# Kernel tuning notes

Hardware: AMD Instinct MI355X
Metric: run time of the kernel (lower is better)

## Reference

```python
import jax, jax.numpy as jnp
import numpy as np

NUM_EMBEDDINGS = 1024
EMBEDDING_DIM = 64
BETA = 0.25


def setup_inputs() -> dict:
    key = jax.random.key(0)
    k1, k2 = jax.random.split(key)
    z = jax.random.normal(k1, (16, EMBEDDING_DIM, 64, 64), dtype=jnp.float32)
    # nn.Embedding weight initialized uniform(-1/K, 1/K)
    embedding = jax.random.uniform(
        k2, (NUM_EMBEDDINGS, EMBEDDING_DIM), dtype=jnp.float32,
        minval=-1.0 / NUM_EMBEDDINGS, maxval=1.0 / NUM_EMBEDDINGS)
    return {"z": z, "embedding": embedding}


def reference(z, embedding):
    # z: [B, C, H, W] -> [B, H, W, C]
    zp = jnp.transpose(z, (0, 2, 3, 1))
    B, H, W, C = zp.shape
    zf = zp.reshape(-1, C)  # [N, C]
    # squared euclidean distances to each codebook entry: [N, K]
    d = (jnp.sum(zf * zf, axis=1, keepdims=True)
         + jnp.sum(embedding * embedding, axis=1)
         - 2.0 * jnp.matmul(zf, embedding.T))
    train_indices = jnp.argmin(d, axis=1)  # [N]
    # gather codebook rows (mathematically identical to one-hot @ embedding)
    z_q = jnp.take(embedding, train_indices, axis=0).reshape(B, H, W, C)
    min_encodings = jax.nn.one_hot(train_indices, NUM_EMBEDDINGS, dtype=jnp.float32)
    embedding_loss = jnp.mean((jax.lax.stop_gradient(z_q) - zp) ** 2)
    q_latent_loss = jnp.mean((z_q - jax.lax.stop_gradient(zp)) ** 2)
    loss = q_latent_loss + BETA * embedding_loss
    # straight-through estimator
    z_q_st = zp + jax.lax.stop_gradient(z_q - zp)
    z_q_out = jnp.transpose(z_q_st, (0, 3, 1, 2))  # back to NCHW
    return loss, z_q_out, min_encodings, train_indices
```

## Files before the change

kernel.cpp:

```cpp
#include <hip/hip_runtime.h>
#include <float.h>


#define K_CODES 1024
#define DIM 64
#define NPTS 65536
#define RANGES 8
#define CPR 128
#define ZQ_OFF 1
#define OH_OFF (1 + 4194304)
#define IDX_OFF (1 + 4194304 + 67108864)
#define ZQ_N 4194304

__device__ __forceinline__ float np_sumsq64(const float* x) {
#pragma clang fp contract(off)
    float t[DIM];
#pragma unroll
    for (int c = 0; c < DIM; ++c) t[c] = x[c] * x[c];
    float r[8];
#pragma unroll
    for (int j = 0; j < 8; ++j) r[j] = t[j];
#pragma unroll
    for (int i = 8; i < DIM; i += 8)
#pragma unroll
        for (int j = 0; j < 8; ++j) r[j] += t[i + j];
    return ((r[0] + r[1]) + (r[2] + r[3])) + ((r[4] + r[5]) + (r[6] + r[7]));
}

__global__ __launch_bounds__(256) void bk_kernel(const float* __restrict__ emb,
                                                 float* __restrict__ bkf) {
    int k = blockIdx.x * 256 + threadIdx.x;
    if (k >= K_CODES) return;
    bkf[k] = np_sumsq64(emb + (size_t)k * DIM);
}

__global__ __launch_bounds__(256) void argmin_partial(
    const float* __restrict__ z, const float* __restrict__ emb,
    const float* __restrict__ bkf,
    float* __restrict__ pscore, int* __restrict__ pidx) {
    int t = threadIdx.x;
    int ptblk = blockIdx.x & 255;
    int range = blockIdx.x >> 8;
    int kbase = range * CPR;

    int n = ptblk * 256 + t;
    int b = n >> 12, hw = n & 4095;
    const float* zb = z + ((size_t)b << 18) + hw;
    float zd[DIM];
#pragma unroll
    for (int c = 0; c < DIM; ++c) zd[c] = zb[(size_t)c << 12];

    float A = np_sumsq64(zd);

    float best = FLT_MAX;
    int bi = kbase;
#pragma unroll 2
    for (int k = 0; k < CPR; ++k) {
        const float4* e4 = (const float4*)(emb + (size_t)(kbase + k) * DIM);
        float m = 0.0f;
#pragma unroll
        for (int i = 0; i < 16; ++i) {
            float4 v = e4[i];
            m = __builtin_fmaf(zd[i * 4 + 0], v.x, m);
            m = __builtin_fmaf(zd[i * 4 + 1], v.y, m);
            m = __builtin_fmaf(zd[i * 4 + 2], v.z, m);
            m = __builtin_fmaf(zd[i * 4 + 3], v.w, m);
        }
        float d;
        {
#pragma clang fp contract(off)
            float t1 = A + bkf[kbase + k];
            d = t1 - 2.0f * m;
        }
        if (d < best) { best = d; bi = kbase + k; }
    }
    pscore[range * NPTS + n] = best;
    pidx[range * NPTS + n] = bi;
}

#define OH_QUADS 16777215
__global__ __launch_bounds__(256) void fill_oh(float* __restrict__ out) {
    const float4 z4 = make_float4(0.f, 0.f, 0.f, 0.f);
    float4* qbase = (float4*)(out + OH_OFF + 3);
    int stride = gridDim.x * 256;
    for (int q = blockIdx.x * 256 + threadIdx.x; q < OH_QUADS; q += stride)
        qbase[q] = z4;
    if (blockIdx.x == 0 && threadIdx.x == 0) {
        out[OH_OFF] = 0.f; out[OH_OFF + 1] = 0.f; out[OH_OFF + 2] = 0.f;
        out[OH_OFF + 67108863] = 0.f;
    }
}

__global__ __launch_bounds__(256) void combine_kernel(
    const float* __restrict__ pscore, const int* __restrict__ pidx,
    int* __restrict__ fidx, float* __restrict__ out) {
    int n = blockIdx.x * 256 + threadIdx.x;
    float best = pscore[n];
    int bi = pidx[n];
#pragma unroll
    for (int r = 1; r < RANGES; ++r) {
        float s = pscore[r * NPTS + n];
        if (s < best) { best = s; bi = pidx[r * NPTS + n]; }
    }
    fidx[n] = bi;
    out[IDX_OFF + n] = (float)bi;
    out[OH_OFF + (size_t)n * K_CODES + bi] = 1.0f;
}

#define ZQ_QUADS 1048575
__global__ __launch_bounds__(256) void zq_loss_kernel(
    const float* __restrict__ z, const float* __restrict__ emb,
    const int* __restrict__ fidx, float* __restrict__ out) {
    int tid = blockIdx.x * 256 + threadIdx.x;
    int stride = gridDim.x * 256;
    float acc = 0.0f;
    for (int q = tid; q < ZQ_QUADS; q += stride) {
        int o = 3 + 4 * q;
        float4 r;
        float* rp = (float*)&r;
#pragma unroll
        for (int j = 0; j < 4; ++j) {
            int oj = o + j;
            int hw = oj & 4095;
            int c = (oj >> 12) & 63;
            int b = oj >> 18;
            int n = (b << 12) | hw;
            float zq = emb[(size_t)fidx[n] * DIM + c];
            float zp = z[oj];
            rp[j] = zp + (zq - zp);
            float d = zq - zp;
            acc = __builtin_fmaf(d, d, acc);
        }
        *(float4*)(out + ZQ_OFF + o) = r;
    }
    if (tid == 0) {
        int extras[4] = {0, 1, 2, 4194303};
#pragma unroll
        for (int e = 0; e < 4; ++e) {
            int oj = extras[e];
            int hw = oj & 4095;
            int c = (oj >> 12) & 63;
            int b = oj >> 18;
            int n = (b << 12) | hw;
            float zq = emb[(size_t)fidx[n] * DIM + c];
            float zp = z[oj];
            out[ZQ_OFF + oj] = zp + (zq - zp);
            float d = zq - zp;
            acc = __builtin_fmaf(d, d, acc);
        }
    }
#pragma unroll
    for (int off = 32; off; off >>= 1) acc += __shfl_down(acc, off, 64);
    __shared__ float wsum[4];
    if ((threadIdx.x & 63) == 0) wsum[threadIdx.x >> 6] = acc;
    __syncthreads();
    if (threadIdx.x == 0) {
        float s = (wsum[0] + wsum[1]) + (wsum[2] + wsum[3]);
        atomicAdd(out, s * (1.25f / 4194304.0f));
    }
}

extern "C" void kernel_launch(void* const* d_in, const int* in_sizes, int n_in,
                              void* d_out, int out_size, void* d_ws, size_t ws_size,
                              hipStream_t stream) {
    const float* z = (const float*)d_in[0];
    const float* emb = (const float*)d_in[1];
    float* out = (float*)d_out;
    char* ws = (char*)d_ws;
    float* bkf = (float*)ws;
    float* pscore = (float*)(ws + 8192);
    int* pidx = (int*)(ws + 8192 + (size_t)RANGES * NPTS * 4);
    int* fidx = (int*)(ws + 8192 + (size_t)RANGES * NPTS * 8);

    hipMemsetAsync(d_out, 0, 4, stream);
    hipLaunchKernelGGL(fill_oh, dim3(2048), dim3(256), 0, stream, out);
    hipLaunchKernelGGL(bk_kernel, dim3(4), dim3(256), 0, stream, emb, bkf);
    hipLaunchKernelGGL(argmin_partial, dim3(256 * RANGES), dim3(256), 0, stream,
                       z, emb, bkf, pscore, pidx);
    hipLaunchKernelGGL(combine_kernel, dim3(NPTS / 256), dim3(256), 0, stream,
                       pscore, pidx, fidx, out);
    hipLaunchKernelGGL(zq_loss_kernel, dim3(1024), dim3(256), 0, stream,
                       z, emb, fidx, out);
}
```

Measured before the change: 572.5 us.

## Fuse one-hot zero fill into combine kernel and block argmin over four codes

The separate one-hot zero-fill kernel is removed. Its work moves into the combine kernel, where each block reduces 64 points and then writes its own 64x1024 one-hot slab, zeros followed by the ones. This avoids a separate pass and the scattered 1.0 writes into memory that was filled earlier. The argmin inner loop now computes four codebook dot products per iteration, raising ILP and reusing the z values across codes, at the cost of higher register pressure.

```diff
diff --git a/kernel.cpp b/kernel.cpp
--- a/kernel.cpp
+++ b/kernel.cpp
@@ -10,7 +10,6 @@
 #define ZQ_OFF 1
 #define OH_OFF (1 + 4194304)
 #define IDX_OFF (1 + 4194304 + 67108864)
-#define ZQ_N 4194304
 
 __device__ __forceinline__ float np_sumsq64(const float* x) {
 #pragma clang fp contract(off)
@@ -54,57 +53,79 @@
 
     float best = FLT_MAX;
     int bi = kbase;
-#pragma unroll 2
-    for (int k = 0; k < CPR; ++k) {
-        const float4* e4 = (const float4*)(emb + (size_t)(kbase + k) * DIM);
-        float m = 0.0f;
+    for (int k = 0; k < CPR; k += 4) {
+        const float4* e0 = (const float4*)(emb + (size_t)(kbase + k + 0) * DIM);
+        const float4* e1 = (const float4*)(emb + (size_t)(kbase + k + 1) * DIM);
+        const float4* e2 = (const float4*)(emb + (size_t)(kbase + k + 2) * DIM);
+        const float4* e3 = (const float4*)(emb + (size_t)(kbase + k + 3) * DIM);
+        float m0 = 0.f, m1 = 0.f, m2 = 0.f, m3 = 0.f;
 #pragma unroll
         for (int i = 0; i < 16; ++i) {
-            float4 v = e4[i];
-            m = __builtin_fmaf(zd[i * 4 + 0], v.x, m);
-            m = __builtin_fmaf(zd[i * 4 + 1], v.y, m);
-            m = __builtin_fmaf(zd[i * 4 + 2], v.z, m);
-            m = __builtin_fmaf(zd[i * 4 + 3], v.w, m);
-        }
-        float d;
+            float4 v0 = e0[i], v1 = e1[i], v2 = e2[i], v3 = e3[i];
+            float za = zd[i * 4 + 0], zbv = zd[i * 4 + 1];
+            float zc = zd[i * 4 + 2], zdv = zd[i * 4 + 3];
+            m0 = __builtin_fmaf(za, v0.x, m0); m0 = __builtin_fmaf(zbv, v0.y, m0);
+            m0 = __builtin_fmaf(zc, v0.z, m0); m0 = __builtin_fmaf(zdv, v0.w, m0);
+            m1 = __builtin_fmaf(za, v1.x, m1); m1 = __builtin_fmaf(zbv, v1.y, m1);
+            m1 = __builtin_fmaf(zc, v1.z, m1); m1 = __builtin_fmaf(zdv, v1.w, m1);
+            m2 = __builtin_fmaf(za, v2.x, m2); m2 = __builtin_fmaf(zbv, v2.y, m2);
+            m2 = __builtin_fmaf(zc, v2.z, m2); m2 = __builtin_fmaf(zdv, v2.w, m2);
+            m3 = __builtin_fmaf(za, v3.x, m3); m3 = __builtin_fmaf(zbv, v3.y, m3);
+            m3 = __builtin_fmaf(zc, v3.z, m3); m3 = __builtin_fmaf(zdv, v3.w, m3);
+        }
+        float d0, d1, d2, d3;
         {
 #pragma clang fp contract(off)
-            float t1 = A + bkf[kbase + k];
-            d = t1 - 2.0f * m;
-        }
-        if (d < best) { best = d; bi = kbase + k; }
+            float t0 = A + bkf[kbase + k + 0]; d0 = t0 - 2.0f * m0;
+            float t1 = A + bkf[kbase + k + 1]; d1 = t1 - 2.0f * m1;
+            float t2 = A + bkf[kbase + k + 2]; d2 = t2 - 2.0f * m2;
+            float t3 = A + bkf[kbase + k + 3]; d3 = t3 - 2.0f * m3;
+        }
+        if (d0 < best) { best = d0; bi = kbase + k + 0; }
+        if (d1 < best) { best = d1; bi = kbase + k + 1; }
+        if (d2 < best) { best = d2; bi = kbase + k + 2; }
+        if (d3 < best) { best = d3; bi = kbase + k + 3; }
     }
     pscore[range * NPTS + n] = best;
     pidx[range * NPTS + n] = bi;
 }
 
-#define OH_QUADS 16777215
-__global__ __launch_bounds__(256) void fill_oh(float* __restrict__ out) {
-    const float4 z4 = make_float4(0.f, 0.f, 0.f, 0.f);
-    float4* qbase = (float4*)(out + OH_OFF + 3);
-    int stride = gridDim.x * 256;
-    for (int q = blockIdx.x * 256 + threadIdx.x; q < OH_QUADS; q += stride)
-        qbase[q] = z4;
-    if (blockIdx.x == 0 && threadIdx.x == 0) {
-        out[OH_OFF] = 0.f; out[OH_OFF + 1] = 0.f; out[OH_OFF + 2] = 0.f;
-        out[OH_OFF + 67108863] = 0.f;
-    }
-}
-
-__global__ __launch_bounds__(256) void combine_kernel(
+__global__ __launch_bounds__(256) void onehot_combine(
     const float* __restrict__ pscore, const int* __restrict__ pidx,
     int* __restrict__ fidx, float* __restrict__ out) {
-    int n = blockIdx.x * 256 + threadIdx.x;
-    float best = pscore[n];
-    int bi = pidx[n];
-#pragma unroll
-    for (int r = 1; r < RANGES; ++r) {
-        float s = pscore[r * NPTS + n];
-        if (s < best) { best = s; bi = pidx[r * NPTS + n]; }
-    }
-    fidx[n] = bi;
-    out[IDX_OFF + n] = (float)bi;
-    out[OH_OFF + (size_t)n * K_CODES + bi] = 1.0f;
+    __shared__ int sbi[64];
+    int t = threadIdx.x;
+    int n0 = blockIdx.x * 64;
+
+    if (t < 64) {
+        int n = n0 + t;
+        float best = pscore[n];
+        int bi = pidx[n];
+#pragma unroll
+        for (int r = 1; r < RANGES; ++r) {
+            float s = pscore[r * NPTS + n];
+            if (s < best) { best = s; bi = pidx[r * NPTS + n]; }
+        }
+        fidx[n] = bi;
+        out[IDX_OFF + n] = (float)bi;
+        sbi[t] = bi;
+    }
+    __syncthreads();
+
+    size_t base = (size_t)OH_OFF + (size_t)n0 * K_CODES;
+    float4* qb = (float4*)(out + base + 3);
+    const float4 z4 = make_float4(0.f, 0.f, 0.f, 0.f);
+#pragma unroll
+    for (int i = 0; i < 64; ++i) {
+        int q = i * 256 + t;
+        if (q < 16383) qb[q] = z4;
+    }
+    if (t == 0) {
+        out[base] = 0.f; out[base + 1] = 0.f; out[base + 2] = 0.f;
+        out[base + 65535] = 0.f;
+    }
+    __syncthreads();
+    if (t < 64) out[base + (size_t)t * K_CODES + sbi[t]] = 1.0f;
 }
 
 #define ZQ_QUADS 1048575
@@ -173,11 +194,10 @@
     int* fidx = (int*)(ws + 8192 + (size_t)RANGES * NPTS * 8);
 
     hipMemsetAsync(d_out, 0, 4, stream);
-    hipLaunchKernelGGL(fill_oh, dim3(2048), dim3(256), 0, stream, out);
     hipLaunchKernelGGL(bk_kernel, dim3(4), dim3(256), 0, stream, emb, bkf);
     hipLaunchKernelGGL(argmin_partial, dim3(256 * RANGES), dim3(256), 0, stream,
                        z, emb, bkf, pscore, pidx);
-    hipLaunchKernelGGL(combine_kernel, dim3(NPTS / 256), dim3(256), 0, stream,
+    hipLaunchKernelGGL(onehot_combine, dim3(NPTS / 64), dim3(256), 0, stream,
                        pscore, pidx, fidx, out);
     hipLaunchKernelGGL(zq_loss_kernel, dim3(1024), dim3(256), 0, stream,
                        z, emb, fidx, out);
```

New measurement: 590.8 us. 1.03x slower.

## Stage codebook slice in LDS and fuse one-hot fill into combine

Applied to the files above, without the earlier changes.

The argmin kernel now copies its 128-code slice of the codebook into shared memory once per block, so the inner loop reads from LDS instead of global/L1. The separate one-hot zero-fill kernel is merged into the combine kernel: each block handles 64 points, zeroes their 64x1024 one-hot rows and then writes the ones after a barrier, which removes one launch and the scattered second write pass. The zq/loss kernel grid is also raised from 1024 to 4096 blocks. The LDS use adds 32KB per block, which may limit occupancy, and the broadcast LDS reads may be no cheaper than the cached global loads.

```diff
diff --git a/kernel.cpp b/kernel.cpp
--- a/kernel.cpp
+++ b/kernel.cpp
@@ -10,7 +10,6 @@
 #define ZQ_OFF 1
 #define OH_OFF (1 + 4194304)
 #define IDX_OFF (1 + 4194304 + 67108864)
-#define ZQ_N 4194304
 
 __device__ __forceinline__ float np_sumsq64(const float* x) {
 #pragma clang fp contract(off)
@@ -38,11 +37,21 @@
     const float* __restrict__ z, const float* __restrict__ emb,
     const float* __restrict__ bkf,
     float* __restrict__ pscore, int* __restrict__ pidx) {
+    __shared__ float se[CPR][DIM];
     int t = threadIdx.x;
     int ptblk = blockIdx.x & 255;
     int range = blockIdx.x >> 8;
     int kbase = range * CPR;
 
+    {
+        const float4* src = (const float4*)(emb + (size_t)kbase * DIM);
+        float4* dst = (float4*)(&se[0][0]);
+#pragma unroll
+        for (int i = 0; i < 8; ++i)
+            dst[t + i * 256] = src[t + i * 256];
+    }
+    __syncthreads();
+
     int n = ptblk * 256 + t;
     int b = n >> 12, hw = n & 4095;
     const float* zb = z + ((size_t)b << 18) + hw;
@@ -56,7 +65,7 @@
     int bi = kbase;
 #pragma unroll 2
     for (int k = 0; k < CPR; ++k) {
-        const float4* e4 = (const float4*)(emb + (size_t)(kbase + k) * DIM);
+        const float4* e4 = (const float4*)(&se[k][0]);
         float m = 0.0f;
 #pragma unroll
         for (int i = 0; i < 16; ++i) {
@@ -78,33 +87,42 @@
     pidx[range * NPTS + n] = bi;
 }
 
-#define OH_QUADS 16777215
-__global__ __launch_bounds__(256) void fill_oh(float* __restrict__ out) {
-    const float4 z4 = make_float4(0.f, 0.f, 0.f, 0.f);
-    float4* qbase = (float4*)(out + OH_OFF + 3);
-    int stride = gridDim.x * 256;
-    for (int q = blockIdx.x * 256 + threadIdx.x; q < OH_QUADS; q += stride)
-        qbase[q] = z4;
-    if (blockIdx.x == 0 && threadIdx.x == 0) {
-        out[OH_OFF] = 0.f; out[OH_OFF + 1] = 0.f; out[OH_OFF + 2] = 0.f;
-        out[OH_OFF + 67108863] = 0.f;
-    }
-}
-
-__global__ __launch_bounds__(256) void combine_kernel(
+__global__ __launch_bounds__(256) void onehot_combine(
     const float* __restrict__ pscore, const int* __restrict__ pidx,
     int* __restrict__ fidx, float* __restrict__ out) {
-    int n = blockIdx.x * 256 + threadIdx.x;
-    float best = pscore[n];
-    int bi = pidx[n];
-#pragma unroll
-    for (int r = 1; r < RANGES; ++r) {
-        float s = pscore[r * NPTS + n];
-        if (s < best) { best = s; bi = pidx[r * NPTS + n]; }
-    }
-    fidx[n] = bi;
-    out[IDX_OFF + n] = (float)bi;
-    out[OH_OFF + (size_t)n * K_CODES + bi] = 1.0f;
+    __shared__ int sbi[64];
+    int t = threadIdx.x;
+    int n0 = blockIdx.x * 64;
+
+    if (t < 64) {
+        int n = n0 + t;
+        float best = pscore[n];
+        int bi = pidx[n];
+#pragma unroll
+        for (int r = 1; r < RANGES; ++r) {
+            float s = pscore[r * NPTS + n];
+            if (s < best) { best = s; bi = pidx[r * NPTS + n]; }
+        }
+        fidx[n] = bi;
+        out[IDX_OFF + n] = (float)bi;
+        sbi[t] = bi;
+    }
+    __syncthreads();
+
+    size_t base = (size_t)OH_OFF + (size_t)n0 * K_CODES;
+    float4* qb = (float4*)(out + base + 3);
+    const float4 z4 = make_float4(0.f, 0.f, 0.f, 0.f);
+#pragma unroll
+    for (int i = 0; i < 64; ++i) {
+        int q = i * 256 + t;
+        if (q < 16383) qb[q] = z4;
+    }
+    if (t == 0) {
+        out[base] = 0.f; out[base + 1] = 0.f; out[base + 2] = 0.f;
+        out[base + 65535] = 0.f;
+    }
+    __syncthreads();
+    if (t < 64) out[base + (size_t)t * K_CODES + sbi[t]] = 1.0f;
 }
 
 #define ZQ_QUADS 1048575
@@ -173,12 +191,11 @@
     int* fidx = (int*)(ws + 8192 + (size_t)RANGES * NPTS * 8);
 
     hipMemsetAsync(d_out, 0, 4, stream);
-    hipLaunchKernelGGL(fill_oh, dim3(2048), dim3(256), 0, stream, out);
     hipLaunchKernelGGL(bk_kernel, dim3(4), dim3(256), 0, stream, emb, bkf);
     hipLaunchKernelGGL(argmin_partial, dim3(256 * RANGES), dim3(256), 0, stream,
                        z, emb, bkf, pscore, pidx);
-    hipLaunchKernelGGL(combine_kernel, dim3(NPTS / 256), dim3(256), 0, stream,
+    hipLaunchKernelGGL(onehot_combine, dim3(NPTS / 64), dim3(256), 0, stream,
                        pscore, pidx, fidx, out);
-    hipLaunchKernelGGL(zq_loss_kernel, dim3(1024), dim3(256), 0, stream,
+    hipLaunchKernelGGL(zq_loss_kernel, dim3(4096), dim3(256), 0, stream,
                        z, emb, fidx, out);
 }
```

Measured after the change: 506.4 us. -11.5%, faster.
